# Kernel tuning notes

Hardware: AMD Instinct MI355X
Metric: run time of the kernel (lower is better)

Reference implementation:

```python
import jax, jax.numpy as jnp
import numpy as np

N_EMBD = 768
N_HEAD = 12
HEAD_DIM = N_EMBD // N_HEAD
N_FREE = 3
NEG = jnp.float32(-1e30)


def _piece_masks():
    """Static 64x64 boolean reachability masks for each chess piece type.
    mask[q, k] = True means query square q may attend to key square k.
    Self-attention (q == k) is always allowed so no row is fully masked."""
    sq = np.arange(64)
    r, c = sq // 8, sq % 8
    dr = r[None, :] - r[:, None]  # row(k) - row(q)
    dc = c[None, :] - c[:, None]
    adr, adc = np.abs(dr), np.abs(dc)
    eye = np.eye(64, dtype=bool)
    knight = ((adr == 1) & (adc == 2)) | ((adr == 2) & (adc == 1))
    bishop = (adr == adc) & (adr != 0)
    rook = ((adr == 0) ^ (adc == 0))
    queen = bishop | rook
    king = np.maximum(adr, adc) == 1
    pawn = (dr == 1) & (adc <= 1)  # one step forward + diagonal captures
    return {k: v | eye for k, v in dict(knight=knight, bishop=bishop, rook=rook,
                                        queen=queen, king=king, pawn=pawn).items()}

_PM = _piece_masks()
# head layout: 2 knight, 2 bishop, 2 rook, 1 queen, 1 king, 1 pawn, 3 free
_PIECE_ORDER = ['knight', 'knight', 'bishop', 'bishop', 'rook', 'rook',
                'queen', 'king', 'pawn']
_PIECE_BIAS = jnp.asarray(
    np.stack([np.where(_PM[p], 0.0, -1e30) for p in _PIECE_ORDER]).astype(np.float32))


def _rmsnorm(x):
    eps = jnp.asarray(jnp.finfo(x.dtype).eps, x.dtype)
    return x * jax.lax.rsqrt(jnp.mean(jnp.square(x), axis=-1, keepdims=True) + eps)


def setup_inputs() -> dict:
    key = jax.random.key(0)
    ks = jax.random.split(key, 6)
    B = 1024
    x = jax.random.normal(ks[0], (B, 64, N_EMBD), dtype=jnp.float32)
    scale = 0.02
    Wq = jax.random.normal(ks[1], (N_EMBD, N_EMBD), dtype=jnp.float32) * scale
    Wk = jax.random.normal(ks[2], (N_EMBD, N_EMBD), dtype=jnp.float32) * scale
    Wv = jax.random.normal(ks[3], (N_EMBD, N_EMBD), dtype=jnp.float32) * scale
    Wo = jax.random.normal(ks[4], (N_EMBD, N_EMBD), dtype=jnp.float32) * scale
    free_logits = jax.random.normal(ks[5], (N_FREE, 64, 64), dtype=jnp.float32) * scale
    return {"x": x, "Wq": Wq, "Wk": Wk, "Wv": Wv, "Wo": Wo,
            "free_logits": free_logits}


def reference(x, Wq, Wk, Wv, Wo, free_logits):
    B, T, C = x.shape  # T == 64
    def proj(W):
        return (x @ W).reshape(B, T, N_HEAD, HEAD_DIM).transpose(0, 2, 1, 3)
    q, k, v = proj(Wq), proj(Wk), proj(Wv)  # (B, H, 64, hd)
    q, k = _rmsnorm(q), _rmsnorm(k)
    # attention bias: fixed piece masks for heads 0..8, learnable log-sigmoid for free heads
    free_bias = jnp.log(jax.nn.sigmoid(free_logits) + 1e-6)  # (3, 64, 64)
    bias = jnp.concatenate([_PIECE_BIAS, free_bias], axis=0)  # (12, 64, 64)
    scale = 1.0 / jnp.sqrt(jnp.asarray(HEAD_DIM, x.dtype))
    scores = jnp.einsum('bhqd,bhkd->bhqk', q, k) * scale + bias[None]
    attn = jax.nn.softmax(scores, axis=-1)
    y = jnp.einsum('bhqk,bhkd->bhqd', attn, v)
    y = y.transpose(0, 2, 1, 3).reshape(B, T, C)
    return y @ Wo
```

## Files before the change

kernel.cpp:

```cpp
#include <hip/hip_runtime.h>
#include <hip/hip_bf16.h>

typedef __attribute__((ext_vector_type(8))) __bf16 bf16x8;
typedef __attribute__((ext_vector_type(4))) float f32x4;
typedef __attribute__((ext_vector_type(8))) unsigned short u16x8;
typedef __attribute__((ext_vector_type(4))) unsigned int u32x4;

#define DEVI static __device__ __forceinline__

DEVI unsigned short f2bf(float f) {
  unsigned u = __builtin_bit_cast(unsigned, f);
  u += 0x7fffu + ((u >> 16) & 1u);
  return (unsigned short)(u >> 16);
}

DEVI bf16x8 ldbf8(const void* p) {
  return __builtin_bit_cast(bf16x8, *(const u16x8*)p);
}

DEVI void gload_lds16(const void* g, void* l) {
  __builtin_amdgcn_global_load_lds(
      (const __attribute__((address_space(1))) void*)g,
      (__attribute__((address_space(3))) void*)l, 16, 0, 0);
}

__global__ __launch_bounds__(256)
void prep_w_kernel(const float* __restrict__ Wq, const float* __restrict__ Wk,
                   const float* __restrict__ Wv, const float* __restrict__ Wo,
                   const float* __restrict__ fl,
                   unsigned short* __restrict__ wqkv,
                   unsigned short* __restrict__ wo_t,
                   float* __restrict__ fb) {
  const int NQKV = 2304 * 768;
  const int NO = 768 * 768;
  int idx = blockIdx.x * 256 + threadIdx.x;
  if (idx < NQKV) {
    int n = idx / 768, kk = idx - n * 768;
    int sel = n / 768;
    int col = n - sel * 768;
    const float* W = (sel == 0) ? Wq : (sel == 1) ? Wk : Wv;
    wqkv[idx] = f2bf(W[kk * 768 + col]);
  } else if (idx < NQKV + NO) {
    int j = idx - NQKV;
    int n = j / 768, kk = j - n * 768;
    wo_t[j] = f2bf(Wo[kk * 768 + n]);
  } else if (idx < NQKV + NO + 3 * 64 * 64) {
    int j = idx - NQKV - NO;
    float v = fl[j];
    fb[j] = logf(1.0f / (1.0f + expf(-v)) + 1e-6f);
  }
}

template <int MODE>
__global__ __launch_bounds__(256, 2)
void gemm_kernel(const float* __restrict__ A32,
                 const unsigned short* __restrict__ Abf,
                 const unsigned short* __restrict__ Bt,
                 unsigned short* __restrict__ q_ws,
                 unsigned short* __restrict__ k_ws,
                 unsigned short* __restrict__ vt_ws,
                 float* __restrict__ out, int nbn) {
  __shared__ __align__(16) unsigned short As[128 * 32];
  __shared__ __align__(16) unsigned short Bs[128 * 32];
  const int tid = threadIdx.x;
  const int lane = tid & 63, wv = tid >> 6;
  const int wr = wv >> 1, wc = wv & 1;
  const int fq = lane >> 4, fr = lane & 15;
  const int bid = blockIdx.x;
  const int bn = bid % nbn, bm = bid / nbn;

  f32x4 acc[4][4];
#pragma unroll
  for (int i = 0; i < 4; ++i)
#pragma unroll
    for (int j = 0; j < 4; ++j)
#pragma unroll
      for (int e = 0; e < 4; ++e) acc[i][j][e] = 0.f;

  for (int kt = 0; kt < 24; ++kt) {
#pragma unroll
    for (int c = 0; c < 2; ++c) {
      int lin = c * 256 + tid;
      int row = lin >> 2;
      int colb = (lin & 3) << 4;
      gload_lds16((const char*)Bt + ((size_t)(bn * 128 + row) * 768 + kt * 32) * 2 + colb,
                  (char*)Bs + c * 4096 + wv * 1024);
    }
    if constexpr (MODE == 0) {
      int row = tid >> 1, half = tid & 1;
      const float4* src =
          (const float4*)(A32 + (size_t)(bm * 128 + row) * 768 + kt * 32 + half * 16);
      float4 a0 = src[0], a1 = src[1], a2 = src[2], a3 = src[3];
      float t0[8] = {a0.x, a0.y, a0.z, a0.w, a1.x, a1.y, a1.z, a1.w};
      float t1[8] = {a2.x, a2.y, a2.z, a2.w, a3.x, a3.y, a3.z, a3.w};
      u16x8 o0, o1;
#pragma unroll
      for (int i = 0; i < 8; ++i) { o0[i] = f2bf(t0[i]); o1[i] = f2bf(t1[i]); }
      *(u16x8*)((char*)As + row * 64 + half * 32) = o0;
      *(u16x8*)((char*)As + row * 64 + half * 32 + 16) = o1;
    } else {
#pragma unroll
      for (int c = 0; c < 2; ++c) {
        int lin = c * 256 + tid;
        int row = lin >> 2;
        int colb = (lin & 3) << 4;
        int m = bm * 128 + row;
        size_t srcb =
            ((size_t)((m >> 6) * 12 + (kt >> 1)) * 4096 + (m & 63) * 64 + (kt & 1) * 32) * 2 +
            colb;
        gload_lds16((const char*)Abf + srcb, (char*)As + c * 4096 + wv * 1024);
      }
    }
    __syncthreads();
    bf16x8 af[4], bfr[4];
#pragma unroll
    for (int i = 0; i < 4; ++i)
      af[i] = ldbf8((const char*)As + (wr * 64 + i * 16 + fr) * 64 + fq * 16);
#pragma unroll
    for (int j = 0; j < 4; ++j)
      bfr[j] = ldbf8((const char*)Bs + (wc * 64 + j * 16 + fr) * 64 + fq * 16);
#pragma unroll
    for (int i = 0; i < 4; ++i)
#pragma unroll
      for (int j = 0; j < 4; ++j)
        acc[i][j] = __builtin_amdgcn_mfma_f32_16x16x32_bf16(af[i], bfr[j], acc[i][j], 0, 0, 0);
    __syncthreads();
  }

  if constexpr (MODE == 0) {
    const int ncb = bn * 128 + wc * 64;
    const int sector = ncb / 768;
    const int hh = (ncb % 768) >> 6;
#pragma unroll
    for (int i = 0; i < 4; ++i) {
      if (sector < 2) {
#pragma unroll
        for (int r = 0; r < 4; ++r) {
          float ss = 0.f;
#pragma unroll
          for (int j = 0; j < 4; ++j) { float v = acc[i][j][r]; ss += v * v; }
          ss += __shfl_xor(ss, 1);
          ss += __shfl_xor(ss, 2);
          ss += __shfl_xor(ss, 4);
          ss += __shfl_xor(ss, 8);
          float rms = rsqrtf(ss * 0.015625f + 1.1920929e-7f);
#pragma unroll
          for (int j = 0; j < 4; ++j) acc[i][j][r] *= rms;
        }
      }
#pragma unroll
      for (int r = 0; r < 4; ++r) {
        int m = bm * 128 + wr * 64 + i * 16 + fq * 4 + r;
        size_t base = (size_t)((m >> 6) * 12 + hh) * 4096;
        int t = m & 63;
#pragma unroll
        for (int j = 0; j < 4; ++j) {
          int d = j * 16 + fr;
          unsigned short v = f2bf(acc[i][j][r]);
          if (sector == 0) q_ws[base + t * 64 + d] = v;
          else if (sector == 1) k_ws[base + t * 64 + d] = v;
          else vt_ws[base + d * 64 + t] = v;
        }
      }
    }
  } else {
#pragma unroll
    for (int i = 0; i < 4; ++i)
#pragma unroll
      for (int r = 0; r < 4; ++r) {
        int m = bm * 128 + wr * 64 + i * 16 + fq * 4 + r;
        float* op = out + (size_t)m * 768 + bn * 128 + wc * 64 + fr;
#pragma unroll
        for (int j = 0; j < 4; ++j) op[j * 16] = acc[i][j][r];
      }
  }
}

DEVI float piece_bias(int h, int tq, int tk) {
  if (tq == tk) return 0.f;
  int rq = tq >> 3, cq = tq & 7;
  int rk = tk >> 3, ck = tk & 7;
  int dr = rk - rq, dc = ck - cq;
  int adr = dr < 0 ? -dr : dr, adc = dc < 0 ? -dc : dc;
  bool ok;
  if (h < 2)       ok = (adr == 1 && adc == 2) || (adr == 2 && adc == 1);
  else if (h < 4)  ok = (adr == adc);
  else if (h < 6)  ok = (adr == 0) != (adc == 0);
  else if (h == 6) ok = (adr == adc) || ((adr == 0) != (adc == 0));
  else if (h == 7) ok = (adr <= 1 && adc <= 1);
  else             ok = (dr == 1) && (adc <= 1);
  return ok ? 0.f : -1e30f;
}

__global__ __launch_bounds__(256, 4)
void attn_kernel(unsigned short* __restrict__ q_ws,
                 const unsigned short* __restrict__ k_ws,
                 const unsigned short* __restrict__ vt_ws,
                 const float* __restrict__ fb) {
  __shared__ __align__(16) unsigned short qs[4096];
  __shared__ __align__(16) unsigned short ks2[4096];
  __shared__ __align__(16) unsigned short vs[4096];
  __shared__ __align__(16) unsigned short ps[4096];
  const int bid = blockIdx.x;
  const int h = bid % 12;
  const int tid = threadIdx.x;
  const int lane = tid & 63, w = tid >> 6;
  const int fq = lane >> 4, fr = lane & 15;
  const size_t gb = (size_t)bid * 8192;

#pragma unroll
  for (int c = 0; c < 2; ++c) {
    int byte = (c * 256 + tid) * 16;
    int row = byte >> 7;
    int colb = byte & 127;
    int sw = (row << 7) | (colb ^ ((row & 7) << 4));
    u32x4 a = *(const u32x4*)((const char*)q_ws + gb + byte);
    u32x4 b = *(const u32x4*)((const char*)k_ws + gb + byte);
    u32x4 v = *(const u32x4*)((const char*)vt_ws + gb + byte);
    *(u32x4*)((char*)qs + sw) = a;
    *(u32x4*)((char*)ks2 + sw) = b;
    *(u32x4*)((char*)vs + sw) = v;
  }
  __syncthreads();

  f32x4 sacc[4];
#pragma unroll
  for (int j = 0; j < 4; ++j)
#pragma unroll
    for (int e = 0; e < 4; ++e) sacc[j][e] = 0.f;
#pragma unroll
  for (int kk = 0; kk < 2; ++kk) {
    int kbyte = kk * 64 + fq * 16;
    int rq = w * 16 + fr;
    bf16x8 af = ldbf8((const char*)qs + (rq << 7) + (kbyte ^ ((rq & 7) << 4)));
#pragma unroll
    for (int j = 0; j < 4; ++j) {
      int rk = j * 16 + fr;
      bf16x8 bf_ = ldbf8((const char*)ks2 + (rk << 7) + (kbyte ^ ((rk & 7) << 4)));
      sacc[j] = __builtin_amdgcn_mfma_f32_16x16x32_bf16(af, bf_, sacc[j], 0, 0, 0);
    }
  }

#pragma unroll
  for (int r = 0; r < 4; ++r) {
    int tq = w * 16 + fq * 4 + r;
    float s[4];
#pragma unroll
    for (int j = 0; j < 4; ++j) {
      int tk = j * 16 + fr;
      float bias = (h >= 9) ? fb[(h - 9) * 4096 + tq * 64 + tk] : piece_bias(h, tq, tk);
      s[j] = sacc[j][r] * 0.125f + bias;
    }
    float mx = fmaxf(fmaxf(s[0], s[1]), fmaxf(s[2], s[3]));
    mx = fmaxf(mx, __shfl_xor(mx, 1));
    mx = fmaxf(mx, __shfl_xor(mx, 2));
    mx = fmaxf(mx, __shfl_xor(mx, 4));
    mx = fmaxf(mx, __shfl_xor(mx, 8));
    float sum = 0.f;
#pragma unroll
    for (int j = 0; j < 4; ++j) { s[j] = __expf(s[j] - mx); sum += s[j]; }
    sum += __shfl_xor(sum, 1);
    sum += __shfl_xor(sum, 2);
    sum += __shfl_xor(sum, 4);
    sum += __shfl_xor(sum, 8);
    float inv = 1.f / sum;
#pragma unroll
    for (int j = 0; j < 4; ++j) {
      int tk = j * 16 + fr;
      *(unsigned short*)((char*)ps + (tq << 7) + ((tk * 2) ^ ((tq & 7) << 4))) =
          f2bf(s[j] * inv);
    }
  }
  __syncthreads();

  f32x4 yacc[4];
#pragma unroll
  for (int j = 0; j < 4; ++j)
#pragma unroll
    for (int e = 0; e < 4; ++e) yacc[j][e] = 0.f;
#pragma unroll
  for (int kk = 0; kk < 2; ++kk) {
    int kbyte = kk * 64 + fq * 16;
    int rp = w * 16 + fr;
    bf16x8 af = ldbf8((const char*)ps + (rp << 7) + (kbyte ^ ((rp & 7) << 4)));
#pragma unroll
    for (int j = 0; j < 4; ++j) {
      int rv = j * 16 + fr;
      bf16x8 bf_ = ldbf8((const char*)vs + (rv << 7) + (kbyte ^ ((rv & 7) << 4)));
      yacc[j] = __builtin_amdgcn_mfma_f32_16x16x32_bf16(af, bf_, yacc[j], 0, 0, 0);
    }
  }
#pragma unroll
  for (int r = 0; r < 4; ++r) {
    int tq = w * 16 + fq * 4 + r;
#pragma unroll
    for (int j = 0; j < 4; ++j) {
      int d = j * 16 + fr;
      q_ws[(size_t)bid * 4096 + tq * 64 + d] = f2bf(yacc[j][r]);
    }
  }
}

extern "C" void kernel_launch(void* const* d_in, const int* in_sizes, int n_in,
                              void* d_out, int out_size, void* d_ws, size_t ws_size,
                              hipStream_t stream) {
  const float* x  = (const float*)d_in[0];
  const float* Wq = (const float*)d_in[1];
  const float* Wk = (const float*)d_in[2];
  const float* Wv = (const float*)d_in[3];
  const float* Wo = (const float*)d_in[4];
  const float* fl = (const float*)d_in[5];
  float* out = (float*)d_out;

  char* ws = (char*)d_ws;
  unsigned short* wqkv = (unsigned short*)ws;
  unsigned short* wo_t = (unsigned short*)(ws + 3538944);
  float* fb = (float*)(ws + 3538944 + 1179648);
  char* big = ws + 3538944 + 1179648 + 49152;
  unsigned short* q_ws  = (unsigned short*)big;
  unsigned short* k_ws  = (unsigned short*)(big + 100663296ULL);
  unsigned short* vt_ws = (unsigned short*)(big + 201326592ULL);

  prep_w_kernel<<<9264, 256, 0, stream>>>(Wq, Wk, Wv, Wo, fl, wqkv, wo_t, fb);
  gemm_kernel<0><<<9216, 256, 0, stream>>>(x, nullptr, wqkv, q_ws, k_ws, vt_ws, nullptr, 18);
  attn_kernel<<<12288, 256, 0, stream>>>(q_ws, k_ws, vt_ws, fb);
  gemm_kernel<1><<<3072, 256, 0, stream>>>(nullptr, q_ws, wo_t, nullptr, nullptr, nullptr, out, 6);
}
```

Measured before the change: 1.030 ms.

## Pre-convert x to bf16, double K-tile with XOR swizzle, remap blocks across XCDs

Adds a separate pass that converts x to bf16 into the output buffer, so the QKV GEMM can load A through direct global-to-LDS copies instead of converting fp32 in-loop. Both GEMMs now use a 64-wide K tile (12 iterations), with an XOR-swizzled LDS layout to avoid bank conflicts. Block IDs are remapped so neighbouring tiles land on the same XCD for better L2 reuse. The trade-off is an extra full read/write pass over x and doubled LDS use per block, which may reduce occupancy.

```diff
diff --git a/kernel.cpp b/kernel.cpp
--- a/kernel.cpp
+++ b/kernel.cpp
@@ -22,6 +22,17 @@
   __builtin_amdgcn_global_load_lds(
       (const __attribute__((address_space(1))) void*)g,
       (__attribute__((address_space(3))) void*)l, 16, 0, 0);
+}
+
+__global__ __launch_bounds__(256)
+void prep_x_kernel(const float* __restrict__ x, unsigned short* __restrict__ xb) {
+  size_t i = (size_t)(blockIdx.x * 256 + threadIdx.x) * 8;
+  const float4* s = (const float4*)(x + i);
+  float4 a = s[0], b = s[1];
+  u16x8 o;
+  o[0] = f2bf(a.x); o[1] = f2bf(a.y); o[2] = f2bf(a.z); o[3] = f2bf(a.w);
+  o[4] = f2bf(b.x); o[5] = f2bf(b.y); o[6] = f2bf(b.z); o[7] = f2bf(b.w);
+  *(u16x8*)(xb + i) = o;
 }
 
 __global__ __launch_bounds__(256)
@@ -53,20 +64,20 @@
 
 template <int MODE>
 __global__ __launch_bounds__(256, 2)
-void gemm_kernel(const float* __restrict__ A32,
-                 const unsigned short* __restrict__ Abf,
+void gemm_kernel(const unsigned short* __restrict__ A,
                  const unsigned short* __restrict__ Bt,
                  unsigned short* __restrict__ q_ws,
                  unsigned short* __restrict__ k_ws,
                  unsigned short* __restrict__ vt_ws,
-                 float* __restrict__ out, int nbn) {
-  __shared__ __align__(16) unsigned short As[128 * 32];
-  __shared__ __align__(16) unsigned short Bs[128 * 32];
+                 float* __restrict__ out, int nbn, int cpx) {
+  __shared__ __align__(16) unsigned short As[128 * 64];
+  __shared__ __align__(16) unsigned short Bs[128 * 64];
   const int tid = threadIdx.x;
   const int lane = tid & 63, wv = tid >> 6;
   const int wr = wv >> 1, wc = wv & 1;
   const int fq = lane >> 4, fr = lane & 15;
-  const int bid = blockIdx.x;
+  const int bid0 = blockIdx.x;
+  const int bid = (bid0 & 7) * cpx + (bid0 >> 3);
   const int bn = bid % nbn, bm = bid / nbn;
 
   f32x4 acc[4][4];
@@ -77,53 +88,43 @@
 #pragma unroll
       for (int e = 0; e < 4; ++e) acc[i][j][e] = 0.f;
 
-  for (int kt = 0; kt < 24; ++kt) {
-#pragma unroll
-    for (int c = 0; c < 2; ++c) {
+  for (int kt = 0; kt < 12; ++kt) {
+#pragma unroll
+    for (int c = 0; c < 4; ++c) {
       int lin = c * 256 + tid;
-      int row = lin >> 2;
-      int colb = (lin & 3) << 4;
-      gload_lds16((const char*)Bt + ((size_t)(bn * 128 + row) * 768 + kt * 32) * 2 + colb,
-                  (char*)Bs + c * 4096 + wv * 1024);
-    }
-    if constexpr (MODE == 0) {
-      int row = tid >> 1, half = tid & 1;
-      const float4* src =
-          (const float4*)(A32 + (size_t)(bm * 128 + row) * 768 + kt * 32 + half * 16);
-      float4 a0 = src[0], a1 = src[1], a2 = src[2], a3 = src[3];
-      float t0[8] = {a0.x, a0.y, a0.z, a0.w, a1.x, a1.y, a1.z, a1.w};
-      float t1[8] = {a2.x, a2.y, a2.z, a2.w, a3.x, a3.y, a3.z, a3.w};
-      u16x8 o0, o1;
-#pragma unroll
-      for (int i = 0; i < 8; ++i) { o0[i] = f2bf(t0[i]); o1[i] = f2bf(t1[i]); }
-      *(u16x8*)((char*)As + row * 64 + half * 32) = o0;
-      *(u16x8*)((char*)As + row * 64 + half * 32 + 16) = o1;
-    } else {
-#pragma unroll
-      for (int c = 0; c < 2; ++c) {
-        int lin = c * 256 + tid;
-        int row = lin >> 2;
-        int colb = (lin & 3) << 4;
+      int row = lin >> 3;
+      int cs = (lin & 7) ^ (row & 7);
+      size_t srcA;
+      if constexpr (MODE == 0) {
+        srcA = ((size_t)(bm * 128 + row) * 1536) + kt * 128 + cs * 16;
+      } else {
         int m = bm * 128 + row;
-        size_t srcb =
-            ((size_t)((m >> 6) * 12 + (kt >> 1)) * 4096 + (m & 63) * 64 + (kt & 1) * 32) * 2 +
-            colb;
-        gload_lds16((const char*)Abf + srcb, (char*)As + c * 4096 + wv * 1024);
-      }
+        srcA = ((size_t)((m >> 6) * 12 + kt) * 8192) + (size_t)(m & 63) * 128 + cs * 16;
+      }
+      gload_lds16((const char*)A + srcA, (char*)As + c * 4096 + wv * 1024);
+      size_t srcB = ((size_t)(bn * 128 + row) * 1536) + kt * 128 + cs * 16;
+      gload_lds16((const char*)Bt + srcB, (char*)Bs + c * 4096 + wv * 1024);
     }
     __syncthreads();
-    bf16x8 af[4], bfr[4];
-#pragma unroll
-    for (int i = 0; i < 4; ++i)
-      af[i] = ldbf8((const char*)As + (wr * 64 + i * 16 + fr) * 64 + fq * 16);
-#pragma unroll
-    for (int j = 0; j < 4; ++j)
-      bfr[j] = ldbf8((const char*)Bs + (wc * 64 + j * 16 + fr) * 64 + fq * 16);
-#pragma unroll
-    for (int i = 0; i < 4; ++i)
-#pragma unroll
-      for (int j = 0; j < 4; ++j)
-        acc[i][j] = __builtin_amdgcn_mfma_f32_16x16x32_bf16(af[i], bfr[j], acc[i][j], 0, 0, 0);
+#pragma unroll
+    for (int kk = 0; kk < 2; ++kk) {
+      bf16x8 af[4], bfr[4];
+#pragma unroll
+      for (int i = 0; i < 4; ++i) {
+        int row = wr * 64 + i * 16 + fr;
+        af[i] = ldbf8((const char*)As + row * 128 + ((kk * 4 + fq) ^ (fr & 7)) * 16);
+      }
+#pragma unroll
+      for (int j = 0; j < 4; ++j) {
+        int row = wc * 64 + j * 16 + fr;
+        bfr[j] = ldbf8((const char*)Bs + row * 128 + ((kk * 4 + fq) ^ (fr & 7)) * 16);
+      }
+#pragma unroll
+      for (int i = 0; i < 4; ++i)
+#pragma unroll
+        for (int j = 0; j < 4; ++j)
+          acc[i][j] = __builtin_amdgcn_mfma_f32_16x16x32_bf16(af[i], bfr[j], acc[i][j], 0, 0, 0);
+    }
     __syncthreads();
   }
 
@@ -320,9 +321,11 @@
   unsigned short* q_ws  = (unsigned short*)big;
   unsigned short* k_ws  = (unsigned short*)(big + 100663296ULL);
   unsigned short* vt_ws = (unsigned short*)(big + 201326592ULL);
-
+  unsigned short* x_bf = (unsigned short*)d_out;
+
+  prep_x_kernel<<<24576, 256, 0, stream>>>(x, x_bf);
   prep_w_kernel<<<9264, 256, 0, stream>>>(Wq, Wk, Wv, Wo, fl, wqkv, wo_t, fb);
-  gemm_kernel<0><<<9216, 256, 0, stream>>>(x, nullptr, wqkv, q_ws, k_ws, vt_ws, nullptr, 18);
+  gemm_kernel<0><<<9216, 256, 0, stream>>>(x_bf, wqkv, q_ws, k_ws, vt_ws, nullptr, 18, 1152);
   attn_kernel<<<12288, 256, 0, stream>>>(q_ws, k_ws, vt_ws, fb);
-  gemm_kernel<1><<<3072, 256, 0, stream>>>(nullptr, q_ws, wo_t, nullptr, nullptr, nullptr, out, 6);
-}
+  gemm_kernel<1><<<3072, 256, 0, stream>>>(q_ws, wo_t, nullptr, nullptr, nullptr, out, 6, 384);
+}
```

Result: faster. 866.6 us (-15.9%).
